# Optimization experiments

Hardware: AMD Instinct MI355X
Metric: run time of the kernel (lower is better)

The kernel has to match this reference:

```python
import jax, jax.numpy as jnp
import numpy as np

B, S, E = 2, 2048, 4096
H, KV, D = 32, 8, 128  # heads, kv heads, head_dim
ROPE_BASE = 500000.0


def setup_inputs() -> dict:
    key = jax.random.key(0)
    ks = jax.random.split(key, 5)
    scale = 0.02
    return {
        "x": jax.random.normal(ks[0], (B, S, E), dtype=jnp.float32),
        "wq": jax.random.normal(ks[1], (E, E), dtype=jnp.float32) * scale,
        "wk": jax.random.normal(ks[2], (KV * D, E), dtype=jnp.float32) * scale,
        "wv": jax.random.normal(ks[3], (KV * D, E), dtype=jnp.float32) * scale,
        "wo": jax.random.normal(ks[4], (E, E), dtype=jnp.float32) * scale,
        "input_pos": jnp.arange(S, dtype=jnp.int64 if jax.config.jax_enable_x64 else jnp.int32),
    }


def _rope(xh, input_pos):
    # xh: [B, H, S, D]; standard llama rotate-half RoPE
    half = D // 2
    inv_freq = 1.0 / (ROPE_BASE ** (jnp.arange(0, half, dtype=jnp.float32) / half))
    ang = input_pos.astype(jnp.float32)[:, None] * inv_freq[None, :]  # [S, half]
    cos, sin = jnp.cos(ang), jnp.sin(ang)
    x1, x2 = xh[..., :half], xh[..., half:]
    return jnp.concatenate([x1 * cos - x2 * sin, x2 * cos + x1 * sin], axis=-1)


def reference(x, wq, wk, wv, wo, input_pos):
    bsz, seq_len, _ = x.shape
    q = (x @ wq.T).reshape(bsz, seq_len, H, D).transpose(0, 2, 1, 3)    # [B,H,S,D]
    k = (x @ wk.T).reshape(bsz, seq_len, KV, D).transpose(0, 2, 1, 3)   # [B,KV,S,D]
    v = (x @ wv.T).reshape(bsz, seq_len, KV, D).transpose(0, 2, 1, 3)
    # repeat_kv: B (H R) S D with R = H // KV
    rep = H // KV
    k = jnp.repeat(k, rep, axis=1)
    v = jnp.repeat(v, rep, axis=1)
    q = _rope(q, input_pos)
    k = _rope(k, input_pos)
    # causal SDPA
    scores = jnp.einsum("bhqd,bhkd->bhqk", q, k) / jnp.sqrt(jnp.float32(D))
    causal = jnp.tril(jnp.ones((seq_len, seq_len), dtype=bool))
    scores = jnp.where(causal, scores, jnp.finfo(scores.dtype).min)
    probs = jax.nn.softmax(scores, axis=-1)
    out = jnp.einsum("bhqk,bhkd->bhqd", probs, v)                       # [B,H,S,D]
    out = out.transpose(0, 2, 1, 3).reshape(bsz, seq_len, E)
    return out @ wo.T
```

## Files before the change

### kernel.cpp

```cpp
#include <hip/hip_runtime.h>

#define B_ 2
#define S_ 2048
#define E_ 4096
#define H_ 32
#define KV_ 8
#define D_ 128

typedef __bf16 v8bf __attribute__((ext_vector_type(8)));
typedef __bf16 v4bf __attribute__((ext_vector_type(4)));
typedef float  v4f  __attribute__((ext_vector_type(4)));

static __device__ __forceinline__ v4f mfma16(v8bf a, v8bf b, v4f c) {
    return __builtin_amdgcn_mfma_f32_16x16x32_bf16(a, b, c, 0, 0, 0);
}

static __device__ __forceinline__ void load_lds16(const void* g, void* l) {
    __builtin_amdgcn_global_load_lds(
        (const __attribute__((address_space(1))) void*)g,
        (__attribute__((address_space(3))) void*)l, 16, 0, 0);
}

__global__ __launch_bounds__(256) void cast_f32_to_bf16(
        const float4* __restrict__ in, v4bf* __restrict__ out, int n4) {
    int i = blockIdx.x * blockDim.x + threadIdx.x;
    if (i >= n4) return;
    float4 v = in[i];
    v4bf o;
    o[0] = (__bf16)v.x; o[1] = (__bf16)v.y; o[2] = (__bf16)v.z; o[3] = (__bf16)v.w;
    out[i] = o;
}

__global__ __launch_bounds__(256) void rope_inplace(
        __bf16* __restrict__ qk, const int* __restrict__ pos, int nh, int rowstride) {
    int idx = blockIdx.x * blockDim.x + threadIdx.x;
    int d = idx & 63;
    int t = idx >> 6;
    int h = t % nh;
    int bs = t / nh;
    if (bs >= B_ * S_) return;
    int s = bs & (S_ - 1);
    float p = (float)pos[s];
    float inv = expf(-(float)d * (1.0f / 64.0f) * 13.122363377404329f);
    float ang = p * inv;
    float c = cosf(ang), sn = sinf(ang);
    size_t off = (size_t)bs * rowstride + (size_t)h * D_;
    float x1 = (float)qk[off + d];
    float x2 = (float)qk[off + d + 64];
    qk[off + d]      = (__bf16)(x1 * c - x2 * sn);
    qk[off + d + 64] = (__bf16)(x2 * c + x1 * sn);
}

template <int EPI>
__global__ __launch_bounds__(512, 2) void gemm_bt(
        const __bf16* __restrict__ A, const __bf16* __restrict__ Bm,
        void* __restrict__ Cv, void* __restrict__ Cv2, int M, int N, int K) {
    __shared__ __bf16 As[2][256 * 64];
    __shared__ __bf16 Bs[2][256 * 64];
    const int tid  = threadIdx.x;
    const int wave = tid >> 6;
    const int lane = tid & 63;
    const int l15  = lane & 15;
    const int quad = lane >> 4;

    const int nbx = N >> 8;
    const int nwg = (int)gridDim.x;
    const int swz = ((int)blockIdx.x & 7) * (nwg >> 3) + ((int)blockIdx.x >> 3);
    const int bm  = (swz / nbx) * 256;
    const int bn  = (swz % nbx) * 256;

    const int wr = wave >> 2;
    const int wc = wave & 3;

    v4f acc[8][4] = {};

    const int srow = wave * 8 + (lane >> 3);
    const int scc  = (lane & 7) ^ ((lane >> 3) & 7);

    auto stage = [&](int t, int buf) {
        const size_t k0 = (size_t)t * 64;
#pragma unroll
        for (int g = 0; g < 4; ++g) {
            load_lds16(A + (size_t)(bm + g * 64 + srow) * K + k0 + scc * 8,
                       (char*)&As[buf][0] + (size_t)g * 8192 + (size_t)wave * 1024);
            load_lds16(Bm + (size_t)(bn + g * 64 + srow) * K + k0 + scc * 8,
                       (char*)&Bs[buf][0] + (size_t)g * 8192 + (size_t)wave * 1024);
        }
    };

    stage(0, 0);

    const int nt = K >> 6;
    for (int t = 0; t < nt; ++t) {
        const int cur = t & 1;
        if (t + 1 < nt) {
            stage(t + 1, cur ^ 1);
            asm volatile("s_waitcnt vmcnt(8)" ::: "memory");
        } else {
            asm volatile("s_waitcnt vmcnt(0)" ::: "memory");
        }
        __builtin_amdgcn_s_barrier();
        __builtin_amdgcn_sched_barrier(0);

        const __bf16* Asc = &As[cur][0];
        const __bf16* Bsc = &Bs[cur][0];
        v8bf a[4][2], b[2][2];

        auto rdA = [&](int mh) {
#pragma unroll
            for (int i = 0; i < 4; ++i)
#pragma unroll
                for (int kk = 0; kk < 2; ++kk)
                    a[i][kk] = *(const v8bf*)&Asc[
                        (wr * 128 + mh * 64 + i * 16 + l15) * 64 +
                        (((kk * 4 + quad) ^ (l15 & 7)) * 8)];
        };
        auto rdB = [&](int nh) {
#pragma unroll
            for (int j = 0; j < 2; ++j)
#pragma unroll
                for (int kk = 0; kk < 2; ++kk)
                    b[j][kk] = *(const v8bf*)&Bsc[
                        (wc * 64 + nh * 32 + j * 16 + l15) * 64 +
                        (((kk * 4 + quad) ^ (l15 & 7)) * 8)];
        };
        auto domfma = [&](int mh, int nh) {
            __builtin_amdgcn_s_setprio(1);
#pragma unroll
            for (int kk = 0; kk < 2; ++kk)
#pragma unroll
                for (int i = 0; i < 4; ++i)
#pragma unroll
                    for (int j = 0; j < 2; ++j)
                        acc[mh * 4 + i][nh * 2 + j] =
                            mfma16(a[i][kk], b[j][kk], acc[mh * 4 + i][nh * 2 + j]);
            __builtin_amdgcn_s_setprio(0);
        };

        rdA(0); rdB(0);
        __builtin_amdgcn_s_barrier();
        domfma(0, 0);
        __builtin_amdgcn_s_barrier();
        __builtin_amdgcn_sched_barrier(0);
        rdB(1);
        __builtin_amdgcn_s_barrier();
        domfma(0, 1);
        __builtin_amdgcn_s_barrier();
        __builtin_amdgcn_sched_barrier(0);
        rdA(1);
        __builtin_amdgcn_s_barrier();
        domfma(1, 1);
        __builtin_amdgcn_s_barrier();
        __builtin_amdgcn_sched_barrier(0);
        rdB(0);
        __builtin_amdgcn_s_barrier();
        domfma(1, 0);
        __builtin_amdgcn_s_barrier();
        __builtin_amdgcn_sched_barrier(0);
    }

#pragma unroll
    for (int mi = 0; mi < 8; ++mi) {
#pragma unroll
        for (int nj = 0; nj < 4; ++nj) {
#pragma unroll
            for (int r = 0; r < 4; ++r) {
                int row = bm + wr * 128 + mi * 16 + quad * 4 + r;
                int col = bn + wc * 64 + nj * 16 + l15;
                float val = acc[mi][nj][r];
                if (EPI == 0) {
                    ((float*)Cv)[(size_t)row * N + col] = val;
                } else if (EPI == 1) {
                    ((__bf16*)Cv)[(size_t)row * N + col] = (__bf16)val;
                } else {
                    if (col < 1024) {
                        ((__bf16*)Cv)[(size_t)row * 1024 + col] = (__bf16)val;
                    } else {
                        int cc = col - 1024;
                        int b  = row >> 11, s = row & (S_ - 1);
                        int kv = cc >> 7,  d = cc & (D_ - 1);
                        ((__bf16*)Cv2)[((size_t)((b * KV_ + kv) * D_ + d)) * S_ + s] = (__bf16)val;
                    }
                }
            }
        }
    }
}

__global__ __launch_bounds__(256, 2) void attn_fused(
        const __bf16* __restrict__ q, const __bf16* __restrict__ k,
        const __bf16* __restrict__ vt, __bf16* __restrict__ attn) {
    __shared__ __bf16 Ks[2][64 * 128];
    __shared__ __bf16 Vs[2][128 * 64];
    __shared__ __bf16 P[4][16 * 72];
    const int wave = threadIdx.x >> 6;
    const int lane = threadIdx.x & 63;

    const int wgid = blockIdx.x;
    const int xcd  = wgid & 7;
    const int slot = wgid >> 3;
    const int bh   = xcd * 8 + (slot >> 5);
    const int qblk = 31 - (slot & 31);
    const int b = bh >> 5;
    const int h = bh & 31;
    const int kvh = h >> 2;
    const int q0 = qblk * 64 + wave * 16;
    const int l15  = lane & 15;
    const int quad = lane >> 4;

    const __bf16* qbase = q  + (size_t)(b * S_) * E_ + (size_t)h * D_;
    const __bf16* kbase = k  + (size_t)(b * S_) * (KV_ * D_) + (size_t)kvh * D_;
    const __bf16* vbase = vt + (size_t)((b * KV_ + kvh) * D_) * S_;
    __bf16* Pw = &P[wave][0];

    const int krow_l = lane >> 4;
    const int kcc    = lane & 15;
    const int vrow_l = lane >> 3;
    const int vcc    = lane & 7;

    auto stageK = [&](int t, int buf) {
#pragma unroll
        for (int i = 0; i < 4; ++i) {
            int g = wave * 4 + i;
            int row = g * 4 + krow_l;
            int scc = kcc ^ (row & 15);
            load_lds16(kbase + (size_t)(t * 64 + row) * (KV_ * D_) + scc * 8,
                       (char*)&Ks[buf][0] + (size_t)g * 1024);
        }
    };
    auto stageV = [&](int t, int buf) {
#pragma unroll
        for (int i = 0; i < 4; ++i) {
            int g = wave * 4 + i;
            int row = g * 8 + vrow_l;
            int scc = vcc ^ (row & 7);
            load_lds16(vbase + (size_t)row * S_ + t * 64 + scc * 8,
                       (char*)&Vs[buf][0] + (size_t)g * 1024);
        }
    };

    stageK(0, 0);
    stageV(0, 0);

    v8bf aq[4];
#pragma unroll
    for (int kc = 0; kc < 4; ++kc)
        aq[kc] = *(const v8bf*)(qbase + (size_t)(q0 + l15) * E_ + kc * 32 + quad * 8);

    v4f o[8] = {};
    float m_i[4], l_i[4];
#pragma unroll
    for (int r = 0; r < 4; ++r) { m_i[r] = -INFINITY; l_i[r] = 0.f; }

    const int ntiles = qblk + 1;
    const int rowbase = q0 + quad * 4;
    const float scale = 0.08838834764831845f;

    for (int t = 0; t < ntiles; ++t) {
        const int cur = t & 1;
        if (t + 1 < ntiles) {
            stageK(t + 1, cur ^ 1);
            stageV(t + 1, cur ^ 1);
            asm volatile("s_waitcnt vmcnt(8)" ::: "memory");
        } else {
            asm volatile("s_waitcnt vmcnt(0)" ::: "memory");
        }
        __builtin_amdgcn_s_barrier();
        __builtin_amdgcn_sched_barrier(0);

        const int n0 = t * 64;
        const __bf16* Ksc = &Ks[cur][0];
        const __bf16* Vsc = &Vs[cur][0];

        v4f s[4] = {};
        __builtin_amdgcn_s_setprio(1);
#pragma unroll
        for (int kc = 0; kc < 4; ++kc) {
            v8bf kf[4];
#pragma unroll
            for (int j = 0; j < 4; ++j)
                kf[j] = *(const v8bf*)&Ksc[(j * 16 + l15) * 128 +
                                           (((kc * 4 + quad) ^ l15) * 8)];
#pragma unroll
            for (int j = 0; j < 4; ++j)
                s[j] = mfma16(aq[kc], kf[j], s[j]);
        }
        __builtin_amdgcn_s_setprio(0);

        float e[4][4];
        if (n0 + 63 > q0) {
#pragma unroll
            for (int j = 0; j < 4; ++j)
#pragma unroll
                for (int r = 0; r < 4; ++r) {
                    float v = s[j][r] * scale;
                    if (n0 + j * 16 + l15 > rowbase + r) v = -INFINITY;
                    e[j][r] = v;
                }
        } else {
#pragma unroll
            for (int j = 0; j < 4; ++j)
#pragma unroll
                for (int r = 0; r < 4; ++r)
                    e[j][r] = s[j][r] * scale;
        }

        float mloc[4];
#pragma unroll
        for (int r = 0; r < 4; ++r)
            mloc[r] = fmaxf(fmaxf(e[0][r], e[1][r]), fmaxf(e[2][r], e[3][r]));
#pragma unroll
        for (int off = 1; off < 16; off <<= 1)
#pragma unroll
            for (int r = 0; r < 4; ++r)
                mloc[r] = fmaxf(mloc[r], __shfl_xor(mloc[r], off, 64));

        float alpha[4], psum[4];
#pragma unroll
        for (int r = 0; r < 4; ++r) {
            float mnew = fmaxf(m_i[r], mloc[r]);
            alpha[r] = __expf(m_i[r] - mnew);
            m_i[r] = mnew;
#pragma unroll
            for (int j = 0; j < 4; ++j)
                e[j][r] = __expf(e[j][r] - mnew);
            psum[r] = (e[0][r] + e[1][r]) + (e[2][r] + e[3][r]);
        }
#pragma unroll
        for (int off = 1; off < 16; off <<= 1)
#pragma unroll
            for (int r = 0; r < 4; ++r)
                psum[r] += __shfl_xor(psum[r], off, 64);
#pragma unroll
        for (int r = 0; r < 4; ++r)
            l_i[r] = l_i[r] * alpha[r] + psum[r];
#pragma unroll
        for (int c = 0; c < 8; ++c)
#pragma unroll
            for (int r = 0; r < 4; ++r)
                o[c][r] *= alpha[r];

#pragma unroll
        for (int j = 0; j < 4; ++j)
#pragma unroll
            for (int r = 0; r < 4; ++r)
                Pw[(quad * 4 + r) * 72 + j * 16 + l15] = (__bf16)e[j][r];

        v8bf ap0 = *(const v8bf*)&Pw[l15 * 72 + quad * 8];
        v8bf ap1 = *(const v8bf*)&Pw[l15 * 72 + 32 + quad * 8];

        __builtin_amdgcn_s_setprio(1);
#pragma unroll
        for (int c = 0; c < 8; ++c) {
            v8bf v0 = *(const v8bf*)&Vsc[(c * 16 + l15) * 64 +
                                         ((quad ^ (l15 & 7)) * 8)];
            v8bf v1 = *(const v8bf*)&Vsc[(c * 16 + l15) * 64 +
                                         (((4 + quad) ^ (l15 & 7)) * 8)];
            o[c] = mfma16(ap0, v0, o[c]);
            o[c] = mfma16(ap1, v1, o[c]);
        }
        __builtin_amdgcn_s_setprio(0);

        __builtin_amdgcn_sched_barrier(0);
        asm volatile("s_waitcnt lgkmcnt(0)" ::: "memory");
        __builtin_amdgcn_s_barrier();
        __builtin_amdgcn_sched_barrier(0);
    }

    float linv[4];
#pragma unroll
    for (int r = 0; r < 4; ++r) linv[r] = 1.0f / l_i[r];
    __bf16* obase = attn + (size_t)(b * S_) * E_ + (size_t)h * D_;
#pragma unroll
    for (int c = 0; c < 8; ++c)
#pragma unroll
        for (int r = 0; r < 4; ++r)
            obase[(size_t)(q0 + quad * 4 + r) * E_ + c * 16 + l15] =
                (__bf16)(o[c][r] * linv[r]);
}

extern "C" void kernel_launch(void* const* d_in, const int* in_sizes, int n_in,
                              void* d_out, int out_size, void* d_ws, size_t ws_size,
                              hipStream_t stream) {
    (void)in_sizes; (void)n_in; (void)out_size; (void)ws_size;
    const float* x  = (const float*)d_in[0];
    const float* wq = (const float*)d_in[1];
    const float* wk = (const float*)d_in[2];
    const float* wv = (const float*)d_in[3];
    const float* wo = (const float*)d_in[4];
    const int*   pos = (const int*)d_in[5];
    float* out = (float*)d_out;

    char* ws = (char*)d_ws;
    size_t off = 0;
    auto alloc = [&](size_t bytes) {
        char* p = ws + off;
        off += (bytes + 255) & ~(size_t)255;
        return p;
    };
    __bf16* xb   = (__bf16*)alloc((size_t)B_ * S_ * E_ * 2);
    __bf16* wqb  = (__bf16*)alloc((size_t)E_ * E_ * 2);
    __bf16* wkvb = (__bf16*)alloc((size_t)2 * KV_ * D_ * E_ * 2);
    __bf16* wob  = (__bf16*)alloc((size_t)E_ * E_ * 2);
    __bf16* qb   = (__bf16*)alloc((size_t)B_ * S_ * E_ * 2);
    __bf16* kb   = (__bf16*)alloc((size_t)B_ * S_ * KV_ * D_ * 2);
    __bf16* vt   = (__bf16*)alloc((size_t)B_ * KV_ * D_ * S_ * 2);
    __bf16* at   = (__bf16*)alloc((size_t)B_ * S_ * E_ * 2);

    auto cast = [&](const float* in, __bf16* ob, size_t n) {
        int n4 = (int)(n / 4);
        cast_f32_to_bf16<<<(n4 + 255) / 256, 256, 0, stream>>>(
            (const float4*)in, (v4bf*)ob, n4);
    };
    cast(x,  xb,  (size_t)B_ * S_ * E_);
    cast(wq, wqb, (size_t)E_ * E_);
    cast(wk, wkvb, (size_t)KV_ * D_ * E_);
    cast(wv, wkvb + (size_t)KV_ * D_ * E_, (size_t)KV_ * D_ * E_);
    cast(wo, wob, (size_t)E_ * E_);

    const int M = B_ * S_;
    const int nwg_e = (E_ / 256) * (M / 256);
    const int nwg_kv = (2 * KV_ * D_ / 256) * (M / 256);
    gemm_bt<1><<<dim3(nwg_e), 512, 0, stream>>>(
        xb, wqb, qb, nullptr, M, E_, E_);
    gemm_bt<2><<<dim3(nwg_kv), 512, 0, stream>>>(
        xb, wkvb, kb, vt, M, 2 * KV_ * D_, E_);

    rope_inplace<<<(B_ * S_ * H_ * 64 + 255) / 256, 256, 0, stream>>>(qb, pos, H_, E_);
    rope_inplace<<<(B_ * S_ * KV_ * 64 + 255) / 256, 256, 0, stream>>>(kb, pos, KV_, KV_ * D_);

    attn_fused<<<dim3(B_ * H_ * (S_ / 64)), 256, 0, stream>>>(qb, kb, vt, at);

    gemm_bt<0><<<dim3(nwg_e), 512, 0, stream>>>(
        at, wob, out, nullptr, M, E_, E_);
}
```

Before: 948.7 us.

## Transpose QK^T MFMA, fold softmax scale into RoPE, add lazy rescaling

The QK^T MFMA operands are swapped so each lane holds scores for a single query row. Row max and sum then need only two cross-quad shuffles instead of four-step butterflies over four rows. The 1/sqrt(D) scale moves into the Q RoPE kernel, and the output rescale is skipped unless some row's max grows by more than 8, following the FlashAttention-4 style lazy rescale. The P tile is now written as packed 4-element vectors into a swizzled LDS layout without padding, which adds bf16 rounding of the prescaled Q and a wave-wide vote branch.

```diff
diff --git a/kernel.cpp b/kernel.cpp
--- a/kernel.cpp
+++ b/kernel.cpp
@@ -32,7 +32,8 @@
 }
 
 __global__ __launch_bounds__(256) void rope_inplace(
-        __bf16* __restrict__ qk, const int* __restrict__ pos, int nh, int rowstride) {
+        __bf16* __restrict__ qk, const int* __restrict__ pos, int nh,
+        int rowstride, float outscale) {
     int idx = blockIdx.x * blockDim.x + threadIdx.x;
     int d = idx & 63;
     int t = idx >> 6;
@@ -47,8 +48,8 @@
     size_t off = (size_t)bs * rowstride + (size_t)h * D_;
     float x1 = (float)qk[off + d];
     float x2 = (float)qk[off + d + 64];
-    qk[off + d]      = (__bf16)(x1 * c - x2 * sn);
-    qk[off + d + 64] = (__bf16)(x2 * c + x1 * sn);
+    qk[off + d]      = (__bf16)((x1 * c - x2 * sn) * outscale);
+    qk[off + d + 64] = (__bf16)((x2 * c + x1 * sn) * outscale);
 }
 
 template <int EPI>
@@ -192,7 +193,7 @@
         const __bf16* __restrict__ vt, __bf16* __restrict__ attn) {
     __shared__ __bf16 Ks[2][64 * 128];
     __shared__ __bf16 Vs[2][128 * 64];
-    __shared__ __bf16 P[4][16 * 72];
+    __shared__ __bf16 P[4][16 * 64];
     const int wave = threadIdx.x >> 6;
     const int lane = threadIdx.x & 63;
 
@@ -248,13 +249,9 @@
         aq[kc] = *(const v8bf*)(qbase + (size_t)(q0 + l15) * E_ + kc * 32 + quad * 8);
 
     v4f o[8] = {};
-    float m_i[4], l_i[4];
-#pragma unroll
-    for (int r = 0; r < 4; ++r) { m_i[r] = -INFINITY; l_i[r] = 0.f; }
+    float m_i = -INFINITY, l_i = 0.f;
 
     const int ntiles = qblk + 1;
-    const int rowbase = q0 + quad * 4;
-    const float scale = 0.08838834764831845f;
 
     for (int t = 0; t < ntiles; ++t) {
         const int cur = t & 1;
@@ -283,7 +280,7 @@
                                            (((kc * 4 + quad) ^ l15) * 8)];
 #pragma unroll
             for (int j = 0; j < 4; ++j)
-                s[j] = mfma16(aq[kc], kf[j], s[j]);
+                s[j] = mfma16(kf[j], aq[kc], s[j]);
         }
         __builtin_amdgcn_s_setprio(0);
 
@@ -293,8 +290,8 @@
             for (int j = 0; j < 4; ++j)
 #pragma unroll
                 for (int r = 0; r < 4; ++r) {
-                    float v = s[j][r] * scale;
-                    if (n0 + j * 16 + l15 > rowbase + r) v = -INFINITY;
+                    float v = s[j][r];
+                    if (n0 + j * 16 + quad * 4 + r > q0 + l15) v = -INFINITY;
                     e[j][r] = v;
                 }
         } else {
@@ -302,52 +299,57 @@
             for (int j = 0; j < 4; ++j)
 #pragma unroll
                 for (int r = 0; r < 4; ++r)
-                    e[j][r] = s[j][r] * scale;
-        }
-
-        float mloc[4];
-#pragma unroll
-        for (int r = 0; r < 4; ++r)
-            mloc[r] = fmaxf(fmaxf(e[0][r], e[1][r]), fmaxf(e[2][r], e[3][r]));
-#pragma unroll
-        for (int off = 1; off < 16; off <<= 1)
+                    e[j][r] = s[j][r];
+        }
+
+        float mloc = e[0][0];
+#pragma unroll
+        for (int j = 0; j < 4; ++j)
 #pragma unroll
             for (int r = 0; r < 4; ++r)
-                mloc[r] = fmaxf(mloc[r], __shfl_xor(mloc[r], off, 64));
-
-        float alpha[4], psum[4];
-#pragma unroll
-        for (int r = 0; r < 4; ++r) {
-            float mnew = fmaxf(m_i[r], mloc[r]);
-            alpha[r] = __expf(m_i[r] - mnew);
-            m_i[r] = mnew;
-#pragma unroll
-            for (int j = 0; j < 4; ++j)
-                e[j][r] = __expf(e[j][r] - mnew);
-            psum[r] = (e[0][r] + e[1][r]) + (e[2][r] + e[3][r]);
-        }
-#pragma unroll
-        for (int off = 1; off < 16; off <<= 1)
+                mloc = fmaxf(mloc, e[j][r]);
+        mloc = fmaxf(mloc, __shfl_xor(mloc, 16, 64));
+        mloc = fmaxf(mloc, __shfl_xor(mloc, 32, 64));
+
+        if (!__all(mloc - m_i <= 8.0f)) {
+            float mnew = fmaxf(m_i, mloc);
+            float alpha = __expf(m_i - mnew);
+            m_i = mnew;
+            l_i *= alpha;
+            float af[4];
 #pragma unroll
             for (int r = 0; r < 4; ++r)
-                psum[r] += __shfl_xor(psum[r], off, 64);
-#pragma unroll
-        for (int r = 0; r < 4; ++r)
-            l_i[r] = l_i[r] * alpha[r] + psum[r];
-#pragma unroll
-        for (int c = 0; c < 8; ++c)
-#pragma unroll
-            for (int r = 0; r < 4; ++r)
-                o[c][r] *= alpha[r];
-
+                af[r] = __shfl(alpha, quad * 4 + r, 16);
+#pragma unroll
+            for (int c = 0; c < 8; ++c)
+#pragma unroll
+                for (int r = 0; r < 4; ++r)
+                    o[c][r] *= af[r];
+        }
+
+        float psum = 0.f;
 #pragma unroll
         for (int j = 0; j < 4; ++j)
 #pragma unroll
-            for (int r = 0; r < 4; ++r)
-                Pw[(quad * 4 + r) * 72 + j * 16 + l15] = (__bf16)e[j][r];
-
-        v8bf ap0 = *(const v8bf*)&Pw[l15 * 72 + quad * 8];
-        v8bf ap1 = *(const v8bf*)&Pw[l15 * 72 + 32 + quad * 8];
+            for (int r = 0; r < 4; ++r) {
+                e[j][r] = __expf(e[j][r] - m_i);
+                psum += e[j][r];
+            }
+        psum += __shfl_xor(psum, 16, 64);
+        psum += __shfl_xor(psum, 32, 64);
+        l_i += psum;
+
+#pragma unroll
+        for (int j = 0; j < 4; ++j) {
+            v4bf pk;
+#pragma unroll
+            for (int r = 0; r < 4; ++r) pk[r] = (__bf16)e[j][r];
+            int cl = j * 2 + (quad >> 1);
+            *(v4bf*)&Pw[l15 * 64 + ((cl ^ (l15 & 7)) << 3) + ((quad & 1) << 2)] = pk;
+        }
+
+        v8bf ap0 = *(const v8bf*)&Pw[l15 * 64 + ((quad ^ (l15 & 7)) << 3)];
+        v8bf ap1 = *(const v8bf*)&Pw[l15 * 64 + (((4 + quad) ^ (l15 & 7)) << 3)];
 
         __builtin_amdgcn_s_setprio(1);
 #pragma unroll
@@ -367,16 +369,18 @@
         __builtin_amdgcn_sched_barrier(0);
     }
 
-    float linv[4];
-#pragma unroll
-    for (int r = 0; r < 4; ++r) linv[r] = 1.0f / l_i[r];
+    float linv = 1.0f / l_i;
+    float lr[4];
+#pragma unroll
+    for (int r = 0; r < 4; ++r)
+        lr[r] = __shfl(linv, quad * 4 + r, 16);
     __bf16* obase = attn + (size_t)(b * S_) * E_ + (size_t)h * D_;
 #pragma unroll
     for (int c = 0; c < 8; ++c)
 #pragma unroll
         for (int r = 0; r < 4; ++r)
             obase[(size_t)(q0 + quad * 4 + r) * E_ + c * 16 + l15] =
-                (__bf16)(o[c][r] * linv[r]);
+                (__bf16)(o[c][r] * lr[r]);
 }
 
 extern "C" void kernel_launch(void* const* d_in, const int* in_sizes, int n_in,
@@ -426,8 +430,10 @@
     gemm_bt<2><<<dim3(nwg_kv), 512, 0, stream>>>(
         xb, wkvb, kb, vt, M, 2 * KV_ * D_, E_);
 
-    rope_inplace<<<(B_ * S_ * H_ * 64 + 255) / 256, 256, 0, stream>>>(qb, pos, H_, E_);
-    rope_inplace<<<(B_ * S_ * KV_ * 64 + 255) / 256, 256, 0, stream>>>(kb, pos, KV_, KV_ * D_);
+    rope_inplace<<<(B_ * S_ * H_ * 64 + 255) / 256, 256, 0, stream>>>(
+        qb, pos, H_, E_, 0.08838834764831845f);
+    rope_inplace<<<(B_ * S_ * KV_ * 64 + 255) / 256, 256, 0, stream>>>(
+        kb, pos, KV_, KV_ * D_, 1.0f);
 
     attn_fused<<<dim3(B_ * H_ * (S_ / 64)), 256, 0, stream>>>(qb, kb, vt, at);
 
```

Measured after the change: 889.1 us. 1.07x faster.
